# Kernel optimization log

Hardware: AMD Instinct MI355X
Metric: run time of the kernel (lower is better)

The kernel has to match this reference:

```python
import jax, jax.numpy as jnp
import numpy as np

H, C, D, F = 8, 1024, 128, 512  # num_heads, num_chanels, out_dim, featurs_dim
B = 16


def setup_inputs() -> dict:
    key = jax.random.key(0)
    ks = jax.random.split(key, 9)
    s = 0.02
    return {
        "x": jax.random.normal(ks[0], (B, C, F), jnp.float32),
        "Wk": jax.random.normal(ks[1], (F, H * D), jnp.float32) * s,
        "bk": jax.random.normal(ks[2], (H * D,), jnp.float32) * s,
        "Wq": jax.random.normal(ks[3], (F, H * D), jnp.float32) * s,
        "bq": jax.random.normal(ks[4], (H * D,), jnp.float32) * s,
        "Wv": jax.random.normal(ks[5], (F, H * D), jnp.float32) * s,
        "bv": jax.random.normal(ks[6], (H * D,), jnp.float32) * s,
        "Ww0": jax.random.normal(ks[7], (H * D, D), jnp.float32) * s,
        "bw0": jax.random.normal(ks[8], (D,), jnp.float32) * s,
    }


def reference(x, Wk, bk, Wq, bq, Wv, bv, Ww0, bw0):
    # Linear projections on last dim: [B, C, H*D]
    # NOTE: the original reshapes [B, C, H*D] -> [B, H, C, D] WITHOUT a permute,
    # which mixes channel/head axes; we replicate that exactly.
    k = (x @ Wk + bk).reshape(-1, H, C, D)
    q = (x @ Wq + bq).reshape(-1, H, C, D)
    v = (x @ Wv + bv).reshape(-1, H, C, D)
    scores = jnp.einsum('bhcf,bhdf->bhcd', q, k) / jnp.sqrt(jnp.float32(D))
    att = jax.nn.softmax(scores, axis=-1) - jnp.eye(C, dtype=scores.dtype)
    vals = jnp.einsum('bhcd,bhdf->bhcf', att, v)          # [B, H, C, D]
    vals = vals.transpose(0, 2, 1, 3).reshape(vals.shape[0], C, H * D)
    return vals @ Ww0 + bw0                                # [B, C, D]
```

## Files before the change

kernel.cpp:

```cpp
#include <hip/hip_runtime.h>
#include <hip/hip_bf16.h>
#include <cstdint>
#include <cstddef>

using u16 = unsigned short;
typedef __attribute__((ext_vector_type(4))) float f32x4;
typedef __attribute__((ext_vector_type(16))) float f32x16;
typedef __attribute__((ext_vector_type(8))) unsigned short u16x8;
typedef __attribute__((ext_vector_type(4))) unsigned short u16x4;
typedef __attribute__((ext_vector_type(4))) unsigned int u32x4;
typedef __bf16 bfrag __attribute__((ext_vector_type(8)));

constexpr int Hn = 8, Cn = 1024, Dn = 128, Fn = 512, Bn = 16;
constexpr int M1 = Bn * Cn;

constexpr size_t OFF_XB  = 0;
constexpr size_t SZ_XB   = (size_t)M1 * Fn * 2;
constexpr size_t OFF_WT  = OFF_XB + SZ_XB;
constexpr size_t SZ_WT   = 3ull * 1024 * 512 * 2;
constexpr size_t OFF_W0T = OFF_WT + SZ_WT;
constexpr size_t SZ_W0T  = 128ull * 1024 * 2;
constexpr size_t OFF_Q   = OFF_W0T + SZ_W0T;
constexpr size_t SZ_P    = (size_t)Bn * Hn * Cn * Dn * 2;
constexpr size_t OFF_K   = OFF_Q + SZ_P;
constexpr size_t OFF_V   = OFF_K + SZ_P;
constexpr size_t OFF_ATT = OFF_V + SZ_P;

__device__ __forceinline__ float bf2f(u16 u) {
  unsigned int x = ((unsigned int)u) << 16;
  return __builtin_bit_cast(float, x);
}
__device__ __forceinline__ u16 f2bf(float f) {
  unsigned int u = __builtin_bit_cast(unsigned int, f);
  u += 0x7fffu + ((u >> 16) & 1u);
  return (u16)(u >> 16);
}
__device__ __forceinline__ f32x4 mfma16(bfrag a, bfrag b, f32x4 c) {
  return __builtin_amdgcn_mfma_f32_16x16x32_bf16(a, b, c, 0, 0, 0);
}
__device__ __forceinline__ f32x16 mfma32(bfrag a, bfrag b, f32x16 c) {
  return __builtin_amdgcn_mfma_f32_32x32x16_bf16(a, b, c, 0, 0, 0);
}
__device__ __forceinline__ void gload16(const void* g, void* lds) {
  __builtin_amdgcn_global_load_lds(
      (const __attribute__((address_space(1))) unsigned int*)g,
      (__attribute__((address_space(3))) unsigned int*)lds, 16, 0, 0);
}
__device__ __forceinline__ unsigned cvtpk(float lo, float hi) {
  unsigned r;
  asm("v_cvt_pk_bf16_f32 %0, %1, %2" : "=v"(r) : "v"(lo), "v"(hi));
  return r;
}
__device__ __forceinline__ float fexp2(float x) {
  float r;
  asm("v_exp_f32 %0, %1" : "=v"(r) : "v"(x));
  return r;
}

__global__ void cvt_bf16(const float* __restrict__ in, u16* __restrict__ out, int n) {
  int idx = (blockIdx.x * blockDim.x + threadIdx.x) * 4;
  if (idx < n) {
    float4 v = *(const float4*)(in + idx);
    u16x4 o;
    o.x = f2bf(v.x); o.y = f2bf(v.y); o.z = f2bf(v.z); o.w = f2bf(v.w);
    *(u16x4*)(out + idx) = o;
  }
}

__global__ void transpose_cvt(const float* __restrict__ in, u16* __restrict__ out,
                              int R, int Cc) {
  __shared__ float tile[32][33];
  int c0 = blockIdx.x * 32, r0 = blockIdx.y * 32;
  int tx = threadIdx.x, ty = threadIdx.y;
#pragma unroll
  for (int i = 0; i < 4; ++i)
    tile[ty + i * 8][tx] = in[(size_t)(r0 + ty + i * 8) * Cc + c0 + tx];
  __syncthreads();
#pragma unroll
  for (int i = 0; i < 4; ++i)
    out[(size_t)(c0 + ty + i * 8) * R + r0 + tx] = f2bf(tile[tx][ty + i * 8]);
}

__global__ void transpose_cvt3(const float* __restrict__ W0, const float* __restrict__ W1,
                               const float* __restrict__ W2, u16* __restrict__ out) {
  __shared__ float tile[32][33];
  const int z = blockIdx.z;
  const float* in = (z == 0) ? W0 : (z == 1) ? W1 : W2;
  u16* op = out + (size_t)z * 1024 * 512;
  int c0 = blockIdx.x * 32, r0 = blockIdx.y * 32;
  int tx = threadIdx.x, ty = threadIdx.y;
#pragma unroll
  for (int i = 0; i < 4; ++i)
    tile[ty + i * 8][tx] = in[(size_t)(r0 + ty + i * 8) * 1024 + c0 + tx];
  __syncthreads();
#pragma unroll
  for (int i = 0; i < 4; ++i)
    op[(size_t)(c0 + ty + i * 8) * 512 + r0 + tx] = f2bf(tile[tx][ty + i * 8]);
}

__global__ void vtrans(const u16* __restrict__ in, u16* __restrict__ out) {
  __shared__ u16 tile[32][33];
  int d0 = blockIdx.x * 32, c0 = blockIdx.y * 32, bh = blockIdx.z;
  const u16* ip = in + (size_t)bh * (Cn * Dn);
  u16* op = out + (size_t)bh * (Dn * Cn);
  int tx = threadIdx.x, ty = threadIdx.y;
#pragma unroll
  for (int i = 0; i < 4; ++i)
    tile[ty + i * 8][tx] = ip[(size_t)(c0 + ty + i * 8) * Dn + d0 + tx];
  __syncthreads();
#pragma unroll
  for (int i = 0; i < 4; ++i)
    op[(size_t)(d0 + ty + i * 8) * Cn + c0 + tx] = tile[tx][ty + i * 8];
}

__global__ __launch_bounds__(512, 1)
void qkv_gemm(const u16* __restrict__ xb, const u16* __restrict__ wt,
              const float* __restrict__ bq, const float* __restrict__ bk,
              const float* __restrict__ bv,
              u16* __restrict__ qout, u16* __restrict__ kout,
              u16* __restrict__ vout) {
  __shared__ u16 smem[3 * 24576];
  char* smb = (char*)smem;

  const int bid = blockIdx.x;
  const int wg = (bid & 7) * 192 + (bid >> 3);
  const int mt = wg / 12, yz = wg % 12;
  const int y = yz / 3, p = yz - y * 3;
  const int m0 = mt * 128, n0 = y * 256;

  const u16* wp = wt + (size_t)p * 1024 * 512;
  const float* bias = (p == 0) ? bq : (p == 1) ? bk : bv;
  u16* outp = (p == 0) ? qout : (p == 1) ? kout : vout;
  const float osc = (p == 0) ? 0.12751744116389548f : 1.0f;

  const int tid = threadIdx.x, l = tid & 63, w = tid >> 6;
  const int lr = l & 15, lg = l >> 4;
  const int wr = w >> 2, wc = w & 3;

  const u16* asrc[2]; unsigned adst[2];
#pragma unroll
  for (int c = 0; c < 2; ++c) {
    int ch = c * 512 + tid, row = ch >> 3, scc = (ch & 7) ^ (row & 7);
    asrc[c] = xb + (size_t)(m0 + row) * 512 + scc * 8;
    adst[c] = (unsigned)(ch * 16);
  }
  const u16* bsrc[4]; unsigned bdst[4];
#pragma unroll
  for (int c = 0; c < 4; ++c) {
    int ch = c * 512 + tid, row = ch >> 3, scc = (ch & 7) ^ (row & 7);
    bsrc[c] = wp + (size_t)(n0 + row) * 512 + scc * 8;
    bdst[c] = (unsigned)(16384 + ch * 16);
  }
  auto stage = [&](int t, int b) {
    char* base = smb + b * 49152;
#pragma unroll
    for (int c = 0; c < 2; ++c) gload16(asrc[c] + t * 64, base + adst[c]);
#pragma unroll
    for (int c = 0; c < 4; ++c) gload16(bsrc[c] + t * 64, base + bdst[c]);
  };

  f32x4 acc[4][4] = {};

  stage(0, 0);
  stage(1, 1);
  asm volatile("s_waitcnt vmcnt(6)" ::: "memory");
  __builtin_amdgcn_s_barrier();

  for (int t = 0; t < 8; ++t) {
    const char* Ab = smb + (t % 3) * 49152;
    const char* Bb = Ab + 16384;
    if (t < 6) stage(t + 2, (t + 2) % 3);

#pragma unroll
    for (int kk = 0; kk < 2; ++kk) {
      bfrag af[4], bf_[4];
#pragma unroll
      for (int fm = 0; fm < 4; ++fm) {
        int row = wr * 64 + fm * 16 + lr;
        af[fm] = *(const bfrag*)(Ab + row * 128 + (((kk * 4 + lg) ^ (row & 7)) * 16));
      }
#pragma unroll
      for (int fn = 0; fn < 4; ++fn) {
        int row = wc * 64 + fn * 16 + lr;
        bf_[fn] = *(const bfrag*)(Bb + row * 128 + (((kk * 4 + lg) ^ (row & 7)) * 16));
      }
      __builtin_amdgcn_s_setprio(1);
#pragma unroll
      for (int fm = 0; fm < 4; ++fm)
#pragma unroll
        for (int fn = 0; fn < 4; ++fn)
          acc[fm][fn] = mfma16(af[fm], bf_[fn], acc[fm][fn]);
      __builtin_amdgcn_s_setprio(0);
    }

    if (t < 6)      asm volatile("s_waitcnt vmcnt(6)" ::: "memory");
    else if (t == 6) asm volatile("s_waitcnt vmcnt(0)" ::: "memory");
    if (t < 7) __builtin_amdgcn_s_barrier();
  }

#pragma unroll
  for (int fm = 0; fm < 4; ++fm) {
#pragma unroll
    for (int r = 0; r < 4; ++r) {
      int m = m0 + wr * 64 + fm * 16 + lg * 4 + r;
      int b = m >> 10, c = m & 1023;
      int gh = c >> 7;
#pragma unroll
      for (int fn = 0; fn < 4; ++fn) {
        int j = n0 + wc * 64 + fn * 16 + lr;
        float v = (acc[fm][fn][r] + bias[j]) * osc;
        int ii = ((c & 127) << 3) | (j >> 7);
        int d = j & 127;
        size_t idx = (((size_t)(b * 8 + gh) * 1024 + ii) << 7) | d;
        outp[idx] = f2bf(v);
      }
    }
  }
}

__global__ __launch_bounds__(512, 2)
void attn_kernel(const u16* __restrict__ qp_all, const u16* __restrict__ kp_all,
                 const u16* __restrict__ vt_all, u16* __restrict__ attout) {
  __shared__ u16 smem[2 * 16384];
  char* smb = (char*)smem;

  const int bid = blockIdx.x;
  const int wg = (bid & 7) * 64 + (bid >> 3);
  const int bh = wg >> 2;
  const int qtp = wg & 3;

  const int tid = threadIdx.x, l = tid & 63, w = tid >> 6;
  const int q31 = l & 31, hi = l >> 5;

  const u16* qp  = qp_all + (size_t)bh * (Cn * Dn);
  const u16* kp  = kp_all + (size_t)bh * (Cn * Dn);
  const u16* vtp = vt_all + (size_t)bh * (Dn * Cn);
  const int qr0 = qtp * 256 + w * 32;

  const unsigned LK = (unsigned)(q31 * 256) ^ (unsigned)((q31 & 15) * 16) ^ (unsigned)(hi * 16);
  const unsigned LV = 16384u ^ (unsigned)(q31 * 128) ^ (unsigned)((q31 & 7) * 16) ^ (unsigned)(hi * 16);

  const u16* ksrc[2]; const u16* vsrc[2];
  unsigned kdst[2], vdst[2];
#pragma unroll
  for (int c = 0; c < 2; ++c) {
    int ch = c * 512 + tid;
    int krow = ch >> 4, kscc = (ch & 15) ^ (krow & 15);
    ksrc[c] = kp + krow * 128 + kscc * 8;
    int vrow = ch >> 3, vscc = (ch & 7) ^ (vrow & 7);
    vsrc[c] = vtp + (size_t)vrow * 1024 + vscc * 8;
    kdst[c] = (unsigned)((c * 512 + w * 64) * 16);
    vdst[c] = 16384u + (unsigned)((c * 512 + w * 64) * 16);
  }
  auto stage = [&](int t2, unsigned bufb) {
#pragma unroll
    for (int c = 0; c < 2; ++c)
      gload16(ksrc[c] + (size_t)t2 * 8192, smb + (bufb ^ kdst[c]));
#pragma unroll
    for (int c = 0; c < 2; ++c)
      gload16(vsrc[c] + (size_t)t2 * 64, smb + (bufb ^ vdst[c]));
  };

  bfrag aq[8];
#pragma unroll
  for (int kk = 0; kk < 8; ++kk)
    aq[kk] = *(const bfrag*)(qp + (size_t)(qr0 + q31) * Dn + kk * 16 + hi * 8);

  f32x16 ot[4] = {};
  float lsum = 0.f;

  stage(0, 0);
  __syncthreads();

  unsigned bufb = 0;
  for (int t = 0; t < 16; ++t) {
    const unsigned nb = bufb ^ 32768u;
    if (t < 15) stage(t + 1, nb);
    const unsigned LKb = LK ^ bufb;
    const unsigned LVb = LV ^ bufb;

    f32x16 st0 = {}, st1 = {};
    __builtin_amdgcn_s_setprio(1);
#pragma unroll
    for (int kk = 0; kk < 8; ++kk) {
      bfrag k0 = *(const bfrag*)(smb + (LKb ^ (unsigned)(kk * 32)));
      st0 = mfma32(k0, aq[kk], st0);
      bfrag k1 = *(const bfrag*)(smb + (LKb ^ (unsigned)(8192 + kk * 32)));
      st1 = mfma32(k1, aq[kk], st1);
    }
    __builtin_amdgcn_s_setprio(0);

    float rp[4] = {0.f, 0.f, 0.f, 0.f};
#pragma unroll
    for (int r = 0; r < 16; ++r) {
      float p0 = fexp2(st0[r]);
      st0[r] = p0;
      rp[r & 3] += p0;
    }
#pragma unroll
    for (int r = 0; r < 16; ++r) {
      float p1 = fexp2(st1[r]);
      st1[r] = p1;
      rp[r & 3] += p1;
    }
    lsum += (rp[0] + rp[1]) + (rp[2] + rp[3]);

    bfrag pb[4];
    {
      unsigned c0_[8], c1_[8];
#pragma unroll
      for (int m = 0; m < 8; ++m) {
        c0_[m] = cvtpk(st0[2 * m], st0[2 * m + 1]);
        c1_[m] = cvtpk(st1[2 * m], st1[2 * m + 1]);
      }
#pragma unroll
      for (int kkt = 0; kkt < 2; ++kkt) {
        unsigned a0 = c0_[4 * kkt + 0], b0 = c0_[4 * kkt + 2];
        unsigned a1 = c0_[4 * kkt + 1], b1 = c0_[4 * kkt + 3];
        asm("v_permlane32_swap_b32 %0, %1" : "+v"(a0), "+v"(b0));
        asm("v_permlane32_swap_b32 %0, %1" : "+v"(a1), "+v"(b1));
        u32x4 bw; bw.x = a0; bw.y = a1; bw.z = b0; bw.w = b1;
        pb[kkt] = __builtin_bit_cast(bfrag, bw);
      }
#pragma unroll
      for (int kkt = 0; kkt < 2; ++kkt) {
        unsigned a0 = c1_[4 * kkt + 0], b0 = c1_[4 * kkt + 2];
        unsigned a1 = c1_[4 * kkt + 1], b1 = c1_[4 * kkt + 3];
        asm("v_permlane32_swap_b32 %0, %1" : "+v"(a0), "+v"(b0));
        asm("v_permlane32_swap_b32 %0, %1" : "+v"(a1), "+v"(b1));
        u32x4 bw; bw.x = a0; bw.y = a1; bw.z = b0; bw.w = b1;
        pb[2 + kkt] = __builtin_bit_cast(bfrag, bw);
      }
    }

    __builtin_amdgcn_s_setprio(1);
#pragma unroll
    for (int kk = 0; kk < 4; ++kk) {
#pragma unroll
      for (int dt = 0; dt < 4; ++dt) {
        bfrag vf = *(const bfrag*)(smb + (LVb ^ (unsigned)(dt * 4096 + kk * 32)));
        ot[dt] = mfma32(vf, pb[kk], ot[dt]);
      }
    }
    __builtin_amdgcn_s_setprio(0);
    __syncthreads();
    bufb = nb;
  }

  const float lfull = lsum + __shfl_xor(lsum, 32, 64);
  const float linv = 1.f / lfull;
  const int c1 = qr0 + q31;
  u16* my = smem + w * 4096;
#pragma unroll
  for (int dt = 0; dt < 4; ++dt)
#pragma unroll
    for (int rp2 = 0; rp2 < 8; ++rp2) {
      int reg = 2 * rp2;
      int d = dt * 32 + (reg & 3) + 8 * (reg >> 2) + 4 * hi;
      float v0 = bf2f(vtp[((size_t)d << 10) | c1]);
      float v1 = bf2f(vtp[((size_t)(d + 1) << 10) | c1]);
      unsigned pk = cvtpk(ot[dt][reg] * linv - v0, ot[dt][reg + 1] * linv - v1);
      *(unsigned*)&my[q31 * 128 + (((d >> 3) ^ (q31 & 7)) << 3) + (d & 7)] = pk;
    }
  const int b = bh >> 3, h = bh & 7;
#pragma unroll
  for (int it = 0; it < 8; ++it) {
    int rowq = it * 4 + (l >> 4);
    int ch = l & 15;
    u16x8 rd = *(const u16x8*)&my[rowq * 128 + ((ch ^ (rowq & 7))) * 8];
    int cg = qr0 + rowq;
    *(u16x8*)&attout[(((size_t)(b * 1024 + cg)) * 8 + h) * 128 + ch * 8] = rd;
  }
}

__global__ void out_gemm(const u16* __restrict__ A, const u16* __restrict__ Bt,
                         const float* __restrict__ bias, float* __restrict__ out) {
  __shared__ u16 As[32 * 64];
  __shared__ u16 Bs[128 * 64];
  const int m0 = blockIdx.x * 32;
  const int tid = threadIdx.x, l = tid & 63, w = tid >> 6;
  const int lr = l & 15, lg = l >> 4;
  f32x4 acc[2][2] = {};

  for (int kt = 0; kt < 1024; kt += 64) {
    {
      int ch = w * 64 + l;
      int row = ch >> 3, scc = (ch & 7) ^ (row & 7);
      gload16(A + (size_t)(m0 + row) * 1024 + kt + scc * 8, &As[(w * 64) * 8]);
    }
#pragma unroll
    for (int i = 0; i < 4; ++i) {
      int chb = (i * 4 + w) * 64;
      int ch = chb + l;
      int row = ch >> 3, scc = (ch & 7) ^ (row & 7);
      gload16(Bt + (size_t)row * 1024 + kt + scc * 8, &Bs[chb * 8]);
    }
    __syncthreads();
#pragma unroll
    for (int kk = 0; kk < 2; ++kk) {
      bfrag af[2], bf_[2];
#pragma unroll
      for (int fm = 0; fm < 2; ++fm) {
        int row = fm * 16 + lr;
        int off = (kk * 4 + lg) ^ (row & 7);
        af[fm] = *(const bfrag*)&As[row * 64 + off * 8];
      }
#pragma unroll
      for (int fn = 0; fn < 2; ++fn) {
        int row = w * 32 + fn * 16 + lr;
        int off = (kk * 4 + lg) ^ (row & 7);
        bf_[fn] = *(const bfrag*)&Bs[row * 64 + off * 8];
      }
#pragma unroll
      for (int fm = 0; fm < 2; ++fm)
#pragma unroll
        for (int fn = 0; fn < 2; ++fn)
          acc[fm][fn] = mfma16(af[fm], bf_[fn], acc[fm][fn]);
    }
    __syncthreads();
  }
#pragma unroll
  for (int fm = 0; fm < 2; ++fm)
#pragma unroll
    for (int r = 0; r < 4; ++r) {
      int m = m0 + fm * 16 + lg * 4 + r;
#pragma unroll
      for (int fn = 0; fn < 2; ++fn) {
        int j = w * 32 + fn * 16 + lr;
        out[(size_t)m * 128 + j] = acc[fm][fn][r] + bias[j];
      }
    }
}

extern "C" void kernel_launch(void* const* d_in, const int* in_sizes, int n_in,
                              void* d_out, int out_size, void* d_ws, size_t ws_size,
                              hipStream_t stream) {
  const float* x   = (const float*)d_in[0];
  const float* Wk  = (const float*)d_in[1];
  const float* bk_ = (const float*)d_in[2];
  const float* Wq  = (const float*)d_in[3];
  const float* bq_ = (const float*)d_in[4];
  const float* Wv  = (const float*)d_in[5];
  const float* bv_ = (const float*)d_in[6];
  const float* Ww0 = (const float*)d_in[7];
  const float* bw0 = (const float*)d_in[8];
  float* out = (float*)d_out;

  char* ws = (char*)d_ws;
  u16* xb   = (u16*)(ws + OFF_XB);
  u16* wt   = (u16*)(ws + OFF_WT);
  u16* w0t  = (u16*)(ws + OFF_W0T);
  u16* qpm  = (u16*)(ws + OFF_Q);
  u16* kpm  = (u16*)(ws + OFF_K);
  u16* vpm  = (u16*)(ws + OFF_V);
  u16* attb = (u16*)(ws + OFF_ATT);

  cvt_bf16<<<(M1 * Fn / 4 + 255) / 256, 256, 0, stream>>>(x, xb, M1 * Fn);
  dim3 tb(32, 8);
  transpose_cvt3<<<dim3(32, 16, 3), tb, 0, stream>>>(Wq, Wk, Wv, wt);
  transpose_cvt<<<dim3(4, 32), tb, 0, stream>>>(Ww0, w0t, 1024, 128);

  qkv_gemm<<<dim3(1536), 512, 0, stream>>>(xb, wt, bq_, bk_, bv_, qpm, kpm, attb);

  vtrans<<<dim3(4, 32, 128), tb, 0, stream>>>(attb, vpm);

  attn_kernel<<<dim3(512), 512, 0, stream>>>(qpm, kpm, vpm, attb);

  out_gemm<<<512, 256, 0, stream>>>(attb, w0t, bw0, out);
}
```

Before: 195.2 us.

## Enlarge QKV GEMM tile to 256x256 with double-buffered interleaved prefetch

The QKV projection GEMM now uses 256x256 output tiles instead of 128x256, so each workgroup computes twice as many rows and the grid is halved. The aim is to cut how often the B (weight) tile is reloaded and to raise MFMA work per LDS byte. The three-stage pipeline is replaced by a two-buffer scheme, with prefetch loads spread across the four compute phases and a __syncthreads per k-step. This doubles the accumulator registers and uses 128KB of LDS. It also drops the explicit vmcnt waits, which may expose load latency and lower occupancy.

Measured after the change: 182.7 us. 6.4% less time.

```diff
diff --git a/kernel.cpp b/kernel.cpp
--- a/kernel.cpp
+++ b/kernel.cpp
@@ -119,14 +119,14 @@
               const float* __restrict__ bv,
               u16* __restrict__ qout, u16* __restrict__ kout,
               u16* __restrict__ vout) {
-  __shared__ u16 smem[3 * 24576];
+  __shared__ u16 smem[2 * 32768];
   char* smb = (char*)smem;
 
   const int bid = blockIdx.x;
-  const int wg = (bid & 7) * 192 + (bid >> 3);
-  const int mt = wg / 12, yz = wg % 12;
-  const int y = yz / 3, p = yz - y * 3;
-  const int m0 = mt * 128, n0 = y * 256;
+  const int wg = (bid & 7) * 96 + (bid >> 3);
+  const int mt = wg / 12, rem = wg % 12;
+  const int y = rem / 3, p = rem - y * 3;
+  const int m0 = mt * 256, n0 = y * 256;
 
   const u16* wp = wt + (size_t)p * 1024 * 512;
   const float* bias = (p == 0) ? bq : (p == 1) ? bk : bv;
@@ -137,72 +137,68 @@
   const int lr = l & 15, lg = l >> 4;
   const int wr = w >> 2, wc = w & 3;
 
-  const u16* asrc[2]; unsigned adst[2];
-#pragma unroll
-  for (int c = 0; c < 2; ++c) {
+  const u16* asrc[4]; const u16* bsrc[4];
+  unsigned adst[4], bdst[4];
+#pragma unroll
+  for (int c = 0; c < 4; ++c) {
     int ch = c * 512 + tid, row = ch >> 3, scc = (ch & 7) ^ (row & 7);
     asrc[c] = xb + (size_t)(m0 + row) * 512 + scc * 8;
+    bsrc[c] = wp + (size_t)(n0 + row) * 512 + scc * 8;
     adst[c] = (unsigned)(ch * 16);
-  }
-  const u16* bsrc[4]; unsigned bdst[4];
-#pragma unroll
-  for (int c = 0; c < 4; ++c) {
-    int ch = c * 512 + tid, row = ch >> 3, scc = (ch & 7) ^ (row & 7);
-    bsrc[c] = wp + (size_t)(n0 + row) * 512 + scc * 8;
-    bdst[c] = (unsigned)(16384 + ch * 16);
-  }
-  auto stage = [&](int t, int b) {
-    char* base = smb + b * 49152;
-#pragma unroll
-    for (int c = 0; c < 2; ++c) gload16(asrc[c] + t * 64, base + adst[c]);
-#pragma unroll
-    for (int c = 0; c < 4; ++c) gload16(bsrc[c] + t * 64, base + bdst[c]);
-  };
-
-  f32x4 acc[4][4] = {};
-
-  stage(0, 0);
-  stage(1, 1);
-  asm volatile("s_waitcnt vmcnt(6)" ::: "memory");
-  __builtin_amdgcn_s_barrier();
+    bdst[c] = (unsigned)(32768 + ch * 16);
+  }
+
+  f32x4 acc[8][4] = {};
+
+  {
+    char* b0 = smb;
+#pragma unroll
+    for (int c = 0; c < 4; ++c) {
+      gload16(asrc[c], b0 + adst[c]);
+      gload16(bsrc[c], b0 + bdst[c]);
+    }
+  }
+  __syncthreads();
 
   for (int t = 0; t < 8; ++t) {
-    const char* Ab = smb + (t % 3) * 49152;
-    const char* Bb = Ab + 16384;
-    if (t < 6) stage(t + 2, (t + 2) % 3);
-
-#pragma unroll
-    for (int kk = 0; kk < 2; ++kk) {
+    const char* cb = smb + (t & 1) * 65536;
+    char* nb = smb + ((t + 1) & 1) * 65536;
+    const bool pre = (t < 7);
+
+#pragma unroll
+    for (int ph = 0; ph < 4; ++ph) {
+      if (pre) {
+        gload16(asrc[ph] + (t + 1) * 64, nb + adst[ph]);
+        gload16(bsrc[ph] + (t + 1) * 64, nb + bdst[ph]);
+      }
+      const int fh = ph >> 1, kk = ph & 1;
       bfrag af[4], bf_[4];
 #pragma unroll
-      for (int fm = 0; fm < 4; ++fm) {
-        int row = wr * 64 + fm * 16 + lr;
-        af[fm] = *(const bfrag*)(Ab + row * 128 + (((kk * 4 + lg) ^ (row & 7)) * 16));
+      for (int fi = 0; fi < 4; ++fi) {
+        int row = wr * 128 + (fh * 4 + fi) * 16 + lr;
+        af[fi] = *(const bfrag*)(cb + row * 128 + (((kk * 4 + lg) ^ (row & 7)) * 16));
       }
 #pragma unroll
       for (int fn = 0; fn < 4; ++fn) {
         int row = wc * 64 + fn * 16 + lr;
-        bf_[fn] = *(const bfrag*)(Bb + row * 128 + (((kk * 4 + lg) ^ (row & 7)) * 16));
+        bf_[fn] = *(const bfrag*)(cb + 32768 + row * 128 + (((kk * 4 + lg) ^ (row & 7)) * 16));
       }
       __builtin_amdgcn_s_setprio(1);
 #pragma unroll
-      for (int fm = 0; fm < 4; ++fm)
+      for (int fi = 0; fi < 4; ++fi)
 #pragma unroll
         for (int fn = 0; fn < 4; ++fn)
-          acc[fm][fn] = mfma16(af[fm], bf_[fn], acc[fm][fn]);
+          acc[fh * 4 + fi][fn] = mfma16(af[fi], bf_[fn], acc[fh * 4 + fi][fn]);
       __builtin_amdgcn_s_setprio(0);
     }
-
-    if (t < 6)      asm volatile("s_waitcnt vmcnt(6)" ::: "memory");
-    else if (t == 6) asm volatile("s_waitcnt vmcnt(0)" ::: "memory");
-    if (t < 7) __builtin_amdgcn_s_barrier();
-  }
-
-#pragma unroll
-  for (int fm = 0; fm < 4; ++fm) {
+    __syncthreads();
+  }
+
+#pragma unroll
+  for (int fm = 0; fm < 8; ++fm) {
 #pragma unroll
     for (int r = 0; r < 4; ++r) {
-      int m = m0 + wr * 64 + fm * 16 + lg * 4 + r;
+      int m = m0 + wr * 128 + fm * 16 + lg * 4 + r;
       int b = m >> 10, c = m & 1023;
       int gh = c >> 7;
 #pragma unroll
@@ -460,7 +456,7 @@
   transpose_cvt3<<<dim3(32, 16, 3), tb, 0, stream>>>(Wq, Wk, Wv, wt);
   transpose_cvt<<<dim3(4, 32), tb, 0, stream>>>(Ww0, w0t, 1024, 128);
 
-  qkv_gemm<<<dim3(1536), 512, 0, stream>>>(xb, wt, bq_, bk_, bv_, qpm, kpm, attb);
+  qkv_gemm<<<dim3(768), 512, 0, stream>>>(xb, wt, bq_, bk_, bv_, qpm, kpm, attb);
 
   vtrans<<<dim3(4, 32, 128), tb, 0, stream>>>(attb, vpm);
 
```
